# Kernel tuning notes

Hardware: AMD Instinct MI355X
Metric: run time of the kernel (lower is better)

## Reference

```python
import jax, jax.numpy as jnp
import numpy as np

N = 100000
K = 20
SCALES = (5, 10, 20)
D = 256  # dimoffeat


def _leaky(x):
    return jax.nn.leaky_relu(x, negative_slope=0.2)


def setup_inputs() -> dict:
    key = jax.random.key(0)
    ks = jax.random.split(key, 20)
    S = len(SCALES)
    inp = {
        "points": jax.random.normal(ks[0], (N, 3), dtype=jnp.float32),
        "neighbor_indices": jax.random.randint(ks[1], (N, K), 0, N, dtype=jnp.int64),
        # per-scale patch PointNet weights, stacked over the 3 scales
        "pw1": jax.random.normal(ks[2], (S, D // 4, 3), dtype=jnp.float32) * 0.05,
        "pb1": jax.random.normal(ks[3], (S, D // 4), dtype=jnp.float32) * 0.05,
        "pw2": jax.random.normal(ks[4], (S, D // 2, D // 4), dtype=jnp.float32) * 0.05,
        "pb2": jax.random.normal(ks[5], (S, D // 2), dtype=jnp.float32) * 0.05,
        "pw3": jax.random.normal(ks[6], (S, D, D // 2), dtype=jnp.float32) * 0.05,
        "pb3": jax.random.normal(ks[7], (S, D), dtype=jnp.float32) * 0.05,
        # shared MLP (all 1x1 convs == linears)
        "sw1": jax.random.normal(ks[8], (D, S * D), dtype=jnp.float32) * 0.05,
        "sb1": jax.random.normal(ks[9], (D,), dtype=jnp.float32) * 0.05,
        "sw2": jax.random.normal(ks[10], (D // 2, D), dtype=jnp.float32) * 0.05,
        "sb2": jax.random.normal(ks[11], (D // 2,), dtype=jnp.float32) * 0.05,
        "sw3": jax.random.normal(ks[12], (D // 4, D // 2), dtype=jnp.float32) * 0.05,
        "sb3": jax.random.normal(ks[13], (D // 4,), dtype=jnp.float32) * 0.05,
        "sw4": jax.random.normal(ks[14], (D // 8, D // 4), dtype=jnp.float32) * 0.05,
        "sb4": jax.random.normal(ks[15], (D // 8,), dtype=jnp.float32) * 0.05,
        "sw5": jax.random.normal(ks[16], (1, D // 8), dtype=jnp.float32) * 0.05,
        "sb5": jax.random.normal(ks[17], (1,), dtype=jnp.float32) * 0.05,
    }
    return inp


def reference(points, pw1, pb1, pw2, pb2, pw3, pb3,
              sw1, sb1, sw2, sb2, sw3, sb3, sw4, sb4, sw5, sb5,
              neighbor_indices):
    feats_list = []
    for i, s in enumerate(SCALES):
        # gather neighbors and center: [N, s, 3]
        nb = points[neighbor_indices[:, :s]] - points[:, None, :]
        # 1x1-conv MLP == per-point linear layers
        h = _leaky(jnp.einsum('nsc,dc->nsd', nb, pw1[i]) + pb1[i])
        h = _leaky(jnp.einsum('nsc,dc->nsd', h, pw2[i]) + pb2[i])
        h = jnp.einsum('nsc,dc->nsd', h, pw3[i]) + pb3[i]
        feats_list.append(jnp.max(h, axis=1))  # max-pool over neighbors -> [N, D]
    x = jnp.concatenate(feats_list, axis=1)  # [N, 3*D]
    h = _leaky(x @ sw1.T + sb1)
    h = _leaky(h @ sw2.T + sb2)
    h = _leaky(h @ sw3.T + sb3)
    h = _leaky(h @ sw4.T + sb4)
    out = h @ sw5.T + sb5  # [N, 1]
    return out[:, 0]
```

## Files before the change

kernel.cpp:

```cpp
#include <hip/hip_runtime.h>


typedef _Float16 f16x8 __attribute__((ext_vector_type(8)));
typedef _Float16 f16x4 __attribute__((ext_vector_type(4)));
typedef __fp16   h16x2 __attribute__((ext_vector_type(2)));
typedef float    f32x4 __attribute__((ext_vector_type(4)));

#define PPB 32
#define KMAX 20

#define PW2OFF 0
#define PW3OFF 24576
#define SW1OFF 122880
#define SW2OFF 319488
#define SW3OFF 352256
#define SW4OFF 360448
#define NFRAGS 708
#define PW1PAD_BYTES 724992

#define NB_OFF 0
#define H1_OFF 10240
#define H2_OFF 33280
#define PW1S_OFF 76800
#define LDS_BYTES 77824
#define H1S 72
#define H2S 136
#define XIS 264
#define X2S 264
#define H3S 136
#define H4S 72
#define O4S 36

__device__ __forceinline__ float leakyf(float x) { return fmaxf(x, 0.2f * x); }

__device__ __forceinline__ f16x4 pkrtz4(f32x4 a) {
    h16x2 lo = __builtin_amdgcn_cvt_pkrtz(a[0], a[1]);
    h16x2 hi = __builtin_amdgcn_cvt_pkrtz(a[2], a[3]);
    f16x4 r;
    r[0] = (_Float16)lo[0]; r[1] = (_Float16)lo[1];
    r[2] = (_Float16)hi[0]; r[3] = (_Float16)hi[1];
    return r;
}
__device__ __forceinline__ f16x4 leaky4h(f16x4 h) {
    f16x4 s = h * (_Float16)0.2f;
    return __builtin_elementwise_max(h, s);
}
__device__ __forceinline__ f16x4 rne4(f32x4 a) {
    f16x4 r; r[0] = (_Float16)a[0]; r[1] = (_Float16)a[1];
    r[2] = (_Float16)a[2]; r[3] = (_Float16)a[3];
    return r;
}
__device__ __forceinline__ f32x4 ldbias4(const float* b) {
    float4 t = *(const float4*)b;
    return (f32x4){t.x, t.y, t.z, t.w};
}

struct PrepRegion { const float* src; int inC; int Kk; int fEnd; int dstOff; };
struct PrepParams {
    PrepRegion r[10];
    const float* pw1; const float* pb1;
    float* pw1pad; _Float16* dst;
};

__global__ __launch_bounds__(256) void prep_kernel(PrepParams pp) {
    int gid = blockIdx.x * 256 + threadIdx.x;
    if (gid < NFRAGS * 64) {
        int f = gid >> 6, L = gid & 63;
        int ri = 0;
        while (f >= pp.r[ri].fEnd) ri++;
        int f0 = (ri == 0) ? 0 : pp.r[ri - 1].fEnd;
        const PrepRegion R = pp.r[ri];
        int fl = f - f0;
        int nt = fl / R.Kk, kk = fl - nt * R.Kk;
        int row = nt * 16 + (L & 15);
        int col = kk * 32 + (L >> 4) * 8;
        const float* s = R.src + row * R.inC + col;
        f16x8 v;
#pragma unroll
        for (int j = 0; j < 8; ++j) v[j] = (_Float16)s[j];
        *(f16x8*)(pp.dst + R.dstOff + fl * 512 + L * 8) = v;
    } else if (gid < NFRAGS * 64 + 192) {
        int t = gid - NFRAGS * 64;
        int i = t >> 6, fd = t & 63;
        float4 w;
        w.x = pp.pw1[i * 192 + fd * 3 + 0];
        w.y = pp.pw1[i * 192 + fd * 3 + 1];
        w.z = pp.pw1[i * 192 + fd * 3 + 2];
        w.w = pp.pb1[i * 64 + fd];
        ((float4*)pp.pw1pad)[i * 64 + fd] = w;
    }
}

struct MainParams {
    const float* points; const int* nidx;
    const float* pb2; const float* pb3;
    const float* sb1; const float* sb2; const float* sb3; const float* sb4;
    const float* sw5; const float* sb5;
    const _Float16* wsH; const float* pw1pad;
    float* out;
    int n;
};

__global__ __launch_bounds__(256, 2) void msp_mfma(MainParams p) {
    __shared__ __align__(16) unsigned char pool[LDS_BYTES];
    float*    nbf = (float*)(pool + NB_OFF);
    _Float16* h1  = (_Float16*)(pool + H1_OFF);
    _Float16* h2  = (_Float16*)(pool + H2_OFF);
    _Float16* xi  = (_Float16*)(pool + H2_OFF);
    _Float16* x2  = (_Float16*)(pool + H1_OFF);
    _Float16* h3  = (_Float16*)(pool + NB_OFF);
    _Float16* h4  = (_Float16*)(pool + H2_OFF);
    float*    out4= (float*)(pool + H2_OFF + 8192);
    float*    pw1s= (float*)(pool + PW1S_OFF);

    const int tid  = threadIdx.x;
    const int wave = tid >> 6, lane = tid & 63;
    const int q = lane >> 4, m16 = lane & 15;
    const int n0 = blockIdx.x * PPB;

    for (int r = tid; r < PPB * KMAX; r += 256) {
        int pp_ = r & 31, k = r >> 5;
        int idx = p.nidx[(n0 + pp_) * KMAX + k];
        const float* npt = p.points + idx * 3;
        const float* cpt = p.points + (n0 + pp_) * 3;
        float4 v;
        v.x = npt[0] - cpt[0];
        v.y = npt[1] - cpt[1];
        v.z = npt[2] - cpt[2];
        v.w = 1.0f;
        ((float4*)nbf)[r] = v;
    }

    f32x4 accC[2][4];
#pragma unroll
    for (int mt = 0; mt < 4; ++mt) {
        f32x4 b = ldbias4(p.sb1 + (wave * 4 + mt) * 16 + q * 4);
        accC[0][mt] = b; accC[1][mt] = b;
    }
    __syncthreads();

    const int NC[3] = {1, 2, 4};
    for (int i = 0; i < 3; ++i) {
        if (tid < 64)
            ((float4*)pw1s)[tid] = ((const float4*)p.pw1pad)[i * 64 + tid];

        f16x8 W2f[2][2], W3f[4][4];
#pragma unroll
        for (int mt = 0; mt < 2; ++mt)
#pragma unroll
            for (int kk = 0; kk < 2; ++kk)
                W2f[mt][kk] = *(const f16x8*)(p.wsH + PW2OFF +
                    (i * 16 + (wave * 2 + mt) * 2 + kk) * 512 + lane * 8);
#pragma unroll
        for (int mt = 0; mt < 4; ++mt)
#pragma unroll
            for (int kk = 0; kk < 4; ++kk)
                W3f[mt][kk] = *(const f16x8*)(p.wsH + PW3OFF +
                    (i * 64 + (wave * 4 + mt) * 4 + kk) * 512 + lane * 8);

        f32x4 b2v[2];
#pragma unroll
        for (int mt = 0; mt < 2; ++mt)
            b2v[mt] = ldbias4(p.pb2 + i * 128 + (wave * 2 + mt) * 16 + q * 4);

        f32x4 maxC[2][4];
#pragma unroll
        for (int pt = 0; pt < 2; ++pt)
#pragma unroll
            for (int mt = 0; mt < 4; ++mt)
                maxC[pt][mt] = (f32x4){-3.0e38f, -3.0e38f, -3.0e38f, -3.0e38f};

        __syncthreads();

        for (int c = 0; c < NC[i]; ++c) {
            const int k0 = c * 5;
            {
                int p_ = tid & 31, g = tid >> 5;
                for (int kc = 0; kc < 5; ++kc) {
                    float4 nv = ((const float4*)nbf)[(k0 + kc) * 32 + p_];
                    f32x4 v0, v1;
#pragma unroll
                    for (int j = 0; j < 4; ++j) {
                        float4 w = ((const float4*)pw1s)[g * 8 + j];
                        v0[j] = leakyf(fmaf(nv.x, w.x, fmaf(nv.y, w.y, fmaf(nv.z, w.z, w.w))));
                    }
#pragma unroll
                    for (int j = 0; j < 4; ++j) {
                        float4 w = ((const float4*)pw1s)[g * 8 + 4 + j];
                        v1[j] = leakyf(fmaf(nv.x, w.x, fmaf(nv.y, w.y, fmaf(nv.z, w.z, w.w))));
                    }
                    f16x4 a = pkrtz4(v0), b = pkrtz4(v1);
                    f16x8 hv;
#pragma unroll
                    for (int j = 0; j < 4; ++j) { hv[j] = a[j]; hv[4 + j] = b[j]; }
                    *(f16x8*)(h1 + (kc * 32 + p_) * H1S + g * 8) = hv;
                }
            }
            __syncthreads();

            for (int nt = 0; nt < 10; ++nt) {
                const _Float16* br = h1 + (nt * 16 + m16) * H1S + q * 8;
                f16x8 b0 = *(const f16x8*)br;
                f16x8 b1 = *(const f16x8*)(br + 32);
                f32x4 acc0 = __builtin_amdgcn_mfma_f32_16x16x32_f16(W2f[0][0], b0, b2v[0], 0, 0, 0);
                f32x4 acc1 = __builtin_amdgcn_mfma_f32_16x16x32_f16(W2f[1][0], b0, b2v[1], 0, 0, 0);
                acc0 = __builtin_amdgcn_mfma_f32_16x16x32_f16(W2f[0][1], b1, acc0, 0, 0, 0);
                acc1 = __builtin_amdgcn_mfma_f32_16x16x32_f16(W2f[1][1], b1, acc1, 0, 0, 0);
                _Float16* wr = h2 + (nt * 16 + m16) * H2S + q * 4;
                *(f16x4*)(wr + (wave * 2 + 0) * 16) = leaky4h(pkrtz4(acc0));
                *(f16x4*)(wr + (wave * 2 + 1) * 16) = leaky4h(pkrtz4(acc1));
            }
            __syncthreads();

            for (int nt = 0; nt < 10; ++nt) {
                const _Float16* br = h2 + (nt * 16 + m16) * H2S + q * 8;
                f16x8 b[4];
#pragma unroll
                for (int kk = 0; kk < 4; ++kk) b[kk] = *(const f16x8*)(br + kk * 32);
                f32x4 acc[4];
#pragma unroll
                for (int mt = 0; mt < 4; ++mt)
                    acc[mt] = __builtin_amdgcn_mfma_f32_16x16x32_f16(W3f[mt][0], b[0],
                              (f32x4){0.f, 0.f, 0.f, 0.f}, 0, 0, 0);
#pragma unroll
                for (int kk = 1; kk < 4; ++kk)
#pragma unroll
                    for (int mt = 0; mt < 4; ++mt)
                        acc[mt] = __builtin_amdgcn_mfma_f32_16x16x32_f16(W3f[mt][kk], b[kk], acc[mt], 0, 0, 0);
                int pt = nt & 1;
#pragma unroll
                for (int mt = 0; mt < 4; ++mt)
                    maxC[pt][mt] = __builtin_elementwise_max(maxC[pt][mt], acc[mt]);
            }
        }

        __syncthreads();
#pragma unroll
        for (int pt = 0; pt < 2; ++pt)
#pragma unroll
            for (int mt = 0; mt < 4; ++mt) {
                f32x4 b3 = ldbias4(p.pb3 + i * 256 + (wave * 4 + mt) * 16 + q * 4);
                *(f16x4*)(xi + (pt * 16 + m16) * XIS + (wave * 4 + mt) * 16 + q * 4)
                    = rne4(maxC[pt][mt] + b3);
            }
        __syncthreads();

        for (int nt = 0; nt < 2; ++nt) {
            const _Float16* br = xi + (nt * 16 + m16) * XIS + q * 8;
            f16x8 bf[8];
#pragma unroll
            for (int kk = 0; kk < 8; ++kk) bf[kk] = *(const f16x8*)(br + kk * 32);
#pragma unroll
            for (int kk = 0; kk < 8; ++kk)
#pragma unroll
                for (int mt = 0; mt < 4; ++mt) {
                    f16x8 a = *(const f16x8*)(p.wsH + SW1OFF +
                        ((wave * 4 + mt) * 24 + i * 8 + kk) * 512 + lane * 8);
                    accC[nt][mt] = __builtin_amdgcn_mfma_f32_16x16x32_f16(a, bf[kk], accC[nt][mt], 0, 0, 0);
                }
        }
    }

#pragma unroll
    for (int nt = 0; nt < 2; ++nt)
#pragma unroll
        for (int mt = 0; mt < 4; ++mt) {
            f32x4 v = accC[nt][mt];
#pragma unroll
            for (int r = 0; r < 4; ++r) v[r] = leakyf(v[r]);
            *(f16x4*)(x2 + (nt * 16 + m16) * X2S + (wave * 4 + mt) * 16 + q * 4) = rne4(v);
        }
    __syncthreads();

    for (int nt = 0; nt < 2; ++nt) {
        const _Float16* br = x2 + (nt * 16 + m16) * X2S + q * 8;
        f16x8 bf[8];
#pragma unroll
        for (int kk = 0; kk < 8; ++kk) bf[kk] = *(const f16x8*)(br + kk * 32);
        f32x4 acc[2];
#pragma unroll
        for (int mt = 0; mt < 2; ++mt)
            acc[mt] = ldbias4(p.sb2 + (wave * 2 + mt) * 16 + q * 4);
#pragma unroll
        for (int kk = 0; kk < 8; ++kk)
#pragma unroll
            for (int mt = 0; mt < 2; ++mt) {
                f16x8 a = *(const f16x8*)(p.wsH + SW2OFF +
                    ((wave * 2 + mt) * 8 + kk) * 512 + lane * 8);
                acc[mt] = __builtin_amdgcn_mfma_f32_16x16x32_f16(a, bf[kk], acc[mt], 0, 0, 0);
            }
#pragma unroll
        for (int mt = 0; mt < 2; ++mt) {
            f32x4 v = acc[mt];
#pragma unroll
            for (int r = 0; r < 4; ++r) v[r] = leakyf(v[r]);
            *(f16x4*)(h3 + (nt * 16 + m16) * H3S + (wave * 2 + mt) * 16 + q * 4) = rne4(v);
        }
    }
    __syncthreads();

    for (int nt = 0; nt < 2; ++nt) {
        const _Float16* br = h3 + (nt * 16 + m16) * H3S + q * 8;
        f32x4 acc = ldbias4(p.sb3 + wave * 16 + q * 4);
#pragma unroll
        for (int kk = 0; kk < 4; ++kk) {
            f16x8 bf = *(const f16x8*)(br + kk * 32);
            f16x8 a = *(const f16x8*)(p.wsH + SW3OFF + (wave * 4 + kk) * 512 + lane * 8);
            acc = __builtin_amdgcn_mfma_f32_16x16x32_f16(a, bf, acc, 0, 0, 0);
        }
#pragma unroll
        for (int r = 0; r < 4; ++r) acc[r] = leakyf(acc[r]);
        *(f16x4*)(h4 + (nt * 16 + m16) * H4S + wave * 16 + q * 4) = rne4(acc);
    }
    __syncthreads();

    if (wave < 2) {
        for (int nt = 0; nt < 2; ++nt) {
            const _Float16* br = h4 + (nt * 16 + m16) * H4S + q * 8;
            f32x4 acc = ldbias4(p.sb4 + wave * 16 + q * 4);
#pragma unroll
            for (int kk = 0; kk < 2; ++kk) {
                f16x8 bf = *(const f16x8*)(br + kk * 32);
                f16x8 a = *(const f16x8*)(p.wsH + SW4OFF + (wave * 2 + kk) * 512 + lane * 8);
                acc = __builtin_amdgcn_mfma_f32_16x16x32_f16(a, bf, acc, 0, 0, 0);
            }
#pragma unroll
            for (int r = 0; r < 4; ++r) acc[r] = leakyf(acc[r]);
            *(f32x4*)(out4 + (nt * 16 + m16) * O4S + wave * 16 + q * 4) = acc;
        }
    }
    __syncthreads();

    if (tid < PPB) {
        float acc = p.sb5[0];
#pragma unroll
        for (int c = 0; c < 32; ++c)
            acc = fmaf(out4[tid * O4S + c], p.sw5[c], acc);
        p.out[n0 + tid] = acc;
    }
}

extern "C" void kernel_launch(void* const* d_in, const int* in_sizes, int n_in,
                              void* d_out, int out_size, void* d_ws, size_t ws_size,
                              hipStream_t stream) {
    const float* points = (const float*)d_in[0];
    const int*   nidx   = (const int*)d_in[1];
    const float* pw1 = (const float*)d_in[2];  const float* pb1 = (const float*)d_in[3];
    const float* pw2 = (const float*)d_in[4];  const float* pb2 = (const float*)d_in[5];
    const float* pw3 = (const float*)d_in[6];  const float* pb3 = (const float*)d_in[7];
    const float* sw1 = (const float*)d_in[8];  const float* sb1 = (const float*)d_in[9];
    const float* sw2 = (const float*)d_in[10]; const float* sb2 = (const float*)d_in[11];
    const float* sw3 = (const float*)d_in[12]; const float* sb3 = (const float*)d_in[13];
    const float* sw4 = (const float*)d_in[14]; const float* sb4 = (const float*)d_in[15];
    const float* sw5 = (const float*)d_in[16]; const float* sb5 = (const float*)d_in[17];

    _Float16* wsH = (_Float16*)d_ws;
    float* pw1pad = (float*)((char*)d_ws + PW1PAD_BYTES);

    PrepParams pp;
    for (int i = 0; i < 3; ++i)
        pp.r[i] = { pw2 + i * 8192, 64, 2, 16 * (i + 1), PW2OFF + i * 8192 };
    for (int i = 0; i < 3; ++i)
        pp.r[3 + i] = { pw3 + i * 32768, 128, 4, 48 + 64 * (i + 1), PW3OFF + i * 32768 };
    pp.r[6] = { sw1, 768, 24, 624, SW1OFF };
    pp.r[7] = { sw2, 256, 8, 688, SW2OFF };
    pp.r[8] = { sw3, 128, 4, 704, SW3OFF };
    pp.r[9] = { sw4, 64, 2, 708, SW4OFF };
    pp.pw1 = pw1; pp.pb1 = pb1;
    pp.pw1pad = pw1pad; pp.dst = wsH;

    int prep_threads = NFRAGS * 64 + 192;
    hipLaunchKernelGGL(prep_kernel, dim3((prep_threads + 255) / 256), dim3(256), 0, stream, pp);

    MainParams mp;
    mp.points = points; mp.nidx = nidx;
    mp.pb2 = pb2; mp.pb3 = pb3;
    mp.sb1 = sb1; mp.sb2 = sb2; mp.sb3 = sb3; mp.sb4 = sb4;
    mp.sw5 = sw5; mp.sb5 = sb5;
    mp.wsH = wsH; mp.pw1pad = pw1pad;
    mp.out = (float*)d_out;
    mp.n = in_sizes[0] / 3;

    int blocks = mp.n / PPB;
    hipLaunchKernelGGL(msp_mfma, dim3(blocks), dim3(256), 0, stream, mp);
}
```

Before: 439.4 us.

## Halve points per block, compute first layer in packed fp16, raise occupancy

Points per block drop from 32 to 16, which roughly halves LDS use and the accumulator registers, and launch bounds are raised to 3 blocks per CU. The first patch layer is now computed with packed fp16 math from an fp16 copy of the pw1/pb1 weights made in the prep kernel, instead of fp32 FMAs. The aim is better latency hiding through occupancy, at the cost of reloading per-scale weight fragments twice as often per point and lower first-layer precision.

```diff
diff --git a/kernel.cpp b/kernel.cpp
--- a/kernel.cpp
+++ b/kernel.cpp
@@ -3,10 +3,11 @@
 
 typedef _Float16 f16x8 __attribute__((ext_vector_type(8)));
 typedef _Float16 f16x4 __attribute__((ext_vector_type(4)));
+typedef _Float16 f16x2 __attribute__((ext_vector_type(2)));
 typedef __fp16   h16x2 __attribute__((ext_vector_type(2)));
 typedef float    f32x4 __attribute__((ext_vector_type(4)));
 
-#define PPB 32
+#define PPB 16
 #define KMAX 20
 
 #define PW2OFF 0
@@ -15,14 +16,14 @@
 #define SW2OFF 319488
 #define SW3OFF 352256
 #define SW4OFF 360448
+#define PW1HOFF 362496
 #define NFRAGS 708
-#define PW1PAD_BYTES 724992
 
 #define NB_OFF 0
-#define H1_OFF 10240
-#define H2_OFF 33280
-#define PW1S_OFF 76800
-#define LDS_BYTES 77824
+#define H1_OFF 5120
+#define H2_OFF 16640
+#define PW1H_OFF 38400
+#define LDS_BYTES 38912
 #define H1S 72
 #define H2S 136
 #define XIS 264
@@ -59,7 +60,7 @@
 struct PrepParams {
     PrepRegion r[10];
     const float* pw1; const float* pb1;
-    float* pw1pad; _Float16* dst;
+    _Float16* dst;
 };
 
 __global__ __launch_bounds__(256) void prep_kernel(PrepParams pp) {
@@ -79,15 +80,20 @@
 #pragma unroll
         for (int j = 0; j < 8; ++j) v[j] = (_Float16)s[j];
         *(f16x8*)(pp.dst + R.dstOff + fl * 512 + L * 8) = v;
-    } else if (gid < NFRAGS * 64 + 192) {
+    } else if (gid < NFRAGS * 64 + 96) {
         int t = gid - NFRAGS * 64;
-        int i = t >> 6, fd = t & 63;
-        float4 w;
-        w.x = pp.pw1[i * 192 + fd * 3 + 0];
-        w.y = pp.pw1[i * 192 + fd * 3 + 1];
-        w.z = pp.pw1[i * 192 + fd * 3 + 2];
-        w.w = pp.pb1[i * 64 + fd];
-        ((float4*)pp.pw1pad)[i * 64 + fd] = w;
+        int i = t >> 5, pr = t & 31;
+        int c0 = pr * 2, c1 = pr * 2 + 1;
+        f16x8 v;
+        v[0] = (_Float16)pp.pw1[i * 192 + c0 * 3 + 0];
+        v[1] = (_Float16)pp.pw1[i * 192 + c1 * 3 + 0];
+        v[2] = (_Float16)pp.pw1[i * 192 + c0 * 3 + 1];
+        v[3] = (_Float16)pp.pw1[i * 192 + c1 * 3 + 1];
+        v[4] = (_Float16)pp.pw1[i * 192 + c0 * 3 + 2];
+        v[5] = (_Float16)pp.pw1[i * 192 + c1 * 3 + 2];
+        v[6] = (_Float16)pp.pb1[i * 64 + c0];
+        v[7] = (_Float16)pp.pb1[i * 64 + c1];
+        *(f16x8*)(pp.dst + PW1HOFF + (i * 32 + pr) * 8) = v;
     }
 }
 
@@ -96,12 +102,12 @@
     const float* pb2; const float* pb3;
     const float* sb1; const float* sb2; const float* sb3; const float* sb4;
     const float* sw5; const float* sb5;
-    const _Float16* wsH; const float* pw1pad;
+    const _Float16* wsH;
     float* out;
     int n;
 };
 
-__global__ __launch_bounds__(256, 2) void msp_mfma(MainParams p) {
+__global__ __launch_bounds__(256, 3) void msp_mfma(MainParams p) {
     __shared__ __align__(16) unsigned char pool[LDS_BYTES];
     float*    nbf = (float*)(pool + NB_OFF);
     _Float16* h1  = (_Float16*)(pool + H1_OFF);
@@ -110,8 +116,8 @@
     _Float16* x2  = (_Float16*)(pool + H1_OFF);
     _Float16* h3  = (_Float16*)(pool + NB_OFF);
     _Float16* h4  = (_Float16*)(pool + H2_OFF);
-    float*    out4= (float*)(pool + H2_OFF + 8192);
-    float*    pw1s= (float*)(pool + PW1S_OFF);
+    float*    out4= (float*)(pool + H2_OFF + 4096);
+    _Float16* pw1h= (_Float16*)(pool + PW1H_OFF);
 
     const int tid  = threadIdx.x;
     const int wave = tid >> 6, lane = tid & 63;
@@ -119,7 +125,7 @@
     const int n0 = blockIdx.x * PPB;
 
     for (int r = tid; r < PPB * KMAX; r += 256) {
-        int pp_ = r & 31, k = r >> 5;
+        int pp_ = r & 15, k = r >> 4;
         int idx = p.nidx[(n0 + pp_) * KMAX + k];
         const float* npt = p.points + idx * 3;
         const float* cpt = p.points + (n0 + pp_) * 3;
@@ -131,18 +137,16 @@
         ((float4*)nbf)[r] = v;
     }
 
-    f32x4 accC[2][4];
-#pragma unroll
-    for (int mt = 0; mt < 4; ++mt) {
-        f32x4 b = ldbias4(p.sb1 + (wave * 4 + mt) * 16 + q * 4);
-        accC[0][mt] = b; accC[1][mt] = b;
-    }
+    f32x4 accC[4];
+#pragma unroll
+    for (int mt = 0; mt < 4; ++mt)
+        accC[mt] = ldbias4(p.sb1 + (wave * 4 + mt) * 16 + q * 4);
     __syncthreads();
 
     const int NC[3] = {1, 2, 4};
     for (int i = 0; i < 3; ++i) {
-        if (tid < 64)
-            ((float4*)pw1s)[tid] = ((const float4*)p.pw1pad)[i * 64 + tid];
+        if (tid < 32)
+            ((f16x8*)pw1h)[tid] = ((const f16x8*)(p.wsH + PW1HOFF))[i * 32 + tid];
 
         f16x8 W2f[2][2], W3f[4][4];
 #pragma unroll
@@ -163,42 +167,44 @@
         for (int mt = 0; mt < 2; ++mt)
             b2v[mt] = ldbias4(p.pb2 + i * 128 + (wave * 2 + mt) * 16 + q * 4);
 
-        f32x4 maxC[2][4];
-#pragma unroll
-        for (int pt = 0; pt < 2; ++pt)
-#pragma unroll
-            for (int mt = 0; mt < 4; ++mt)
-                maxC[pt][mt] = (f32x4){-3.0e38f, -3.0e38f, -3.0e38f, -3.0e38f};
+        f32x4 maxC[4];
+#pragma unroll
+        for (int mt = 0; mt < 4; ++mt)
+            maxC[mt] = (f32x4){-3.0e38f, -3.0e38f, -3.0e38f, -3.0e38f};
 
         __syncthreads();
 
         for (int c = 0; c < NC[i]; ++c) {
             const int k0 = c * 5;
             {
-                int p_ = tid & 31, g = tid >> 5;
-                for (int kc = 0; kc < 5; ++kc) {
-                    float4 nv = ((const float4*)nbf)[(k0 + kc) * 32 + p_];
-                    f32x4 v0, v1;
-#pragma unroll
-                    for (int j = 0; j < 4; ++j) {
-                        float4 w = ((const float4*)pw1s)[g * 8 + j];
-                        v0[j] = leakyf(fmaf(nv.x, w.x, fmaf(nv.y, w.y, fmaf(nv.z, w.z, w.w))));
+                int p_ = tid & 15;
+                int g  = (tid >> 4) & 7;
+                int kh = tid >> 7;
+                for (int kc = 0; kc < 5; kc += 2) {
+                    int k = kc + kh;
+                    if (k < 5) {
+                        float4 nv = ((const float4*)nbf)[(k0 + k) * 16 + p_];
+                        f16x2 X; X[0] = X[1] = (_Float16)nv.x;
+                        f16x2 Y; Y[0] = Y[1] = (_Float16)nv.y;
+                        f16x2 Z; Z[0] = Z[1] = (_Float16)nv.z;
+                        f16x8 hv;
+#pragma unroll
+                        for (int j = 0; j < 4; ++j) {
+                            f16x8 w8 = ((const f16x8*)pw1h)[g * 4 + j];
+                            f16x2 wx = {w8[0], w8[1]}, wy = {w8[2], w8[3]};
+                            f16x2 wz = {w8[4], w8[5]}, wb = {w8[6], w8[7]};
+                            f16x2 v = wx * X + wy * Y + wz * Z + wb;
+                            f16x2 s = v * (_Float16)0.2f;
+                            v = __builtin_elementwise_max(v, s);
+                            hv[2 * j] = v[0]; hv[2 * j + 1] = v[1];
+                        }
+                        *(f16x8*)(h1 + (k * 16 + p_) * H1S + g * 8) = hv;
                     }
-#pragma unroll
-                    for (int j = 0; j < 4; ++j) {
-                        float4 w = ((const float4*)pw1s)[g * 8 + 4 + j];
-                        v1[j] = leakyf(fmaf(nv.x, w.x, fmaf(nv.y, w.y, fmaf(nv.z, w.z, w.w))));
-                    }
-                    f16x4 a = pkrtz4(v0), b = pkrtz4(v1);
-                    f16x8 hv;
-#pragma unroll
-                    for (int j = 0; j < 4; ++j) { hv[j] = a[j]; hv[4 + j] = b[j]; }
-                    *(f16x8*)(h1 + (kc * 32 + p_) * H1S + g * 8) = hv;
                 }
             }
             __syncthreads();
 
-            for (int nt = 0; nt < 10; ++nt) {
+            for (int nt = 0; nt < 5; ++nt) {
                 const _Float16* br = h1 + (nt * 16 + m16) * H1S + q * 8;
                 f16x8 b0 = *(const f16x8*)br;
                 f16x8 b1 = *(const f16x8*)(br + 32);
@@ -212,7 +218,7 @@
             }
             __syncthreads();
 
-            for (int nt = 0; nt < 10; ++nt) {
+            for (int nt = 0; nt < 5; ++nt) {
                 const _Float16* br = h2 + (nt * 16 + m16) * H2S + q * 8;
                 f16x8 b[4];
 #pragma unroll
@@ -227,26 +233,23 @@
 #pragma unroll
                     for (int mt = 0; mt < 4; ++mt)
                         acc[mt] = __builtin_amdgcn_mfma_f32_16x16x32_f16(W3f[mt][kk], b[kk], acc[mt], 0, 0, 0);
-                int pt = nt & 1;
 #pragma unroll
                 for (int mt = 0; mt < 4; ++mt)
-                    maxC[pt][mt] = __builtin_elementwise_max(maxC[pt][mt], acc[mt]);
+                    maxC[mt] = __builtin_elementwise_max(maxC[mt], acc[mt]);
             }
         }
 
         __syncthreads();
 #pragma unroll
-        for (int pt = 0; pt < 2; ++pt)
-#pragma unroll
-            for (int mt = 0; mt < 4; ++mt) {
-                f32x4 b3 = ldbias4(p.pb3 + i * 256 + (wave * 4 + mt) * 16 + q * 4);
-                *(f16x4*)(xi + (pt * 16 + m16) * XIS + (wave * 4 + mt) * 16 + q * 4)
-                    = rne4(maxC[pt][mt] + b3);
-            }
+        for (int mt = 0; mt < 4; ++mt) {
+            f32x4 b3 = ldbias4(p.pb3 + i * 256 + (wave * 4 + mt) * 16 + q * 4);
+            *(f16x4*)(xi + m16 * XIS + (wave * 4 + mt) * 16 + q * 4)
+                = rne4(maxC[mt] + b3);
+        }
         __syncthreads();
 
-        for (int nt = 0; nt < 2; ++nt) {
-            const _Float16* br = xi + (nt * 16 + m16) * XIS + q * 8;
+        {
+            const _Float16* br = xi + m16 * XIS + q * 8;
             f16x8 bf[8];
 #pragma unroll
             for (int kk = 0; kk < 8; ++kk) bf[kk] = *(const f16x8*)(br + kk * 32);
@@ -256,24 +259,22 @@
                 for (int mt = 0; mt < 4; ++mt) {
                     f16x8 a = *(const f16x8*)(p.wsH + SW1OFF +
                         ((wave * 4 + mt) * 24 + i * 8 + kk) * 512 + lane * 8);
-                    accC[nt][mt] = __builtin_amdgcn_mfma_f32_16x16x32_f16(a, bf[kk], accC[nt][mt], 0, 0, 0);
+                    accC[mt] = __builtin_amdgcn_mfma_f32_16x16x32_f16(a, bf[kk], accC[mt], 0, 0, 0);
                 }
         }
     }
 
 #pragma unroll
-    for (int nt = 0; nt < 2; ++nt)
-#pragma unroll
-        for (int mt = 0; mt < 4; ++mt) {
-            f32x4 v = accC[nt][mt];
-#pragma unroll
-            for (int r = 0; r < 4; ++r) v[r] = leakyf(v[r]);
-            *(f16x4*)(x2 + (nt * 16 + m16) * X2S + (wave * 4 + mt) * 16 + q * 4) = rne4(v);
-        }
-    __syncthreads();
-
-    for (int nt = 0; nt < 2; ++nt) {
-        const _Float16* br = x2 + (nt * 16 + m16) * X2S + q * 8;
+    for (int mt = 0; mt < 4; ++mt) {
+        f32x4 v = accC[mt];
+#pragma unroll
+        for (int r = 0; r < 4; ++r) v[r] = leakyf(v[r]);
+        *(f16x4*)(x2 + m16 * X2S + (wave * 4 + mt) * 16 + q * 4) = rne4(v);
+    }
+    __syncthreads();
+
+    {
+        const _Float16* br = x2 + m16 * X2S + q * 8;
         f16x8 bf[8];
 #pragma unroll
         for (int kk = 0; kk < 8; ++kk) bf[kk] = *(const f16x8*)(br + kk * 32);
@@ -294,13 +295,13 @@
             f32x4 v = acc[mt];
 #pragma unroll
             for (int r = 0; r < 4; ++r) v[r] = leakyf(v[r]);
-            *(f16x4*)(h3 + (nt * 16 + m16) * H3S + (wave * 2 + mt) * 16 + q * 4) = rne4(v);
-        }
-    }
-    __syncthreads();
-
-    for (int nt = 0; nt < 2; ++nt) {
-        const _Float16* br = h3 + (nt * 16 + m16) * H3S + q * 8;
+            *(f16x4*)(h3 + m16 * H3S + (wave * 2 + mt) * 16 + q * 4) = rne4(v);
+        }
+    }
+    __syncthreads();
+
+    {
+        const _Float16* br = h3 + m16 * H3S + q * 8;
         f32x4 acc = ldbias4(p.sb3 + wave * 16 + q * 4);
 #pragma unroll
         for (int kk = 0; kk < 4; ++kk) {
@@ -310,24 +311,22 @@
         }
 #pragma unroll
         for (int r = 0; r < 4; ++r) acc[r] = leakyf(acc[r]);
-        *(f16x4*)(h4 + (nt * 16 + m16) * H4S + wave * 16 + q * 4) = rne4(acc);
+        *(f16x4*)(h4 + m16 * H4S + wave * 16 + q * 4) = rne4(acc);
     }
     __syncthreads();
 
     if (wave < 2) {
-        for (int nt = 0; nt < 2; ++nt) {
-            const _Float16* br = h4 + (nt * 16 + m16) * H4S + q * 8;
-            f32x4 acc = ldbias4(p.sb4 + wave * 16 + q * 4);
-#pragma unroll
-            for (int kk = 0; kk < 2; ++kk) {
-                f16x8 bf = *(const f16x8*)(br + kk * 32);
-                f16x8 a = *(const f16x8*)(p.wsH + SW4OFF + (wave * 2 + kk) * 512 + lane * 8);
-                acc = __builtin_amdgcn_mfma_f32_16x16x32_f16(a, bf, acc, 0, 0, 0);
-            }
-#pragma unroll
-            for (int r = 0; r < 4; ++r) acc[r] = leakyf(acc[r]);
-            *(f32x4*)(out4 + (nt * 16 + m16) * O4S + wave * 16 + q * 4) = acc;
-        }
+        const _Float16* br = h4 + m16 * H4S + q * 8;
+        f32x4 acc = ldbias4(p.sb4 + wave * 16 + q * 4);
+#pragma unroll
+        for (int kk = 0; kk < 2; ++kk) {
+            f16x8 bf = *(const f16x8*)(br + kk * 32);
+            f16x8 a = *(const f16x8*)(p.wsH + SW4OFF + (wave * 2 + kk) * 512 + lane * 8);
+            acc = __builtin_amdgcn_mfma_f32_16x16x32_f16(a, bf, acc, 0, 0, 0);
+        }
+#pragma unroll
+        for (int r = 0; r < 4; ++r) acc[r] = leakyf(acc[r]);
+        *(f32x4*)(out4 + m16 * O4S + wave * 16 + q * 4) = acc;
     }
     __syncthreads();
 
@@ -355,7 +354,6 @@
     const float* sw5 = (const float*)d_in[16]; const float* sb5 = (const float*)d_in[17];
 
     _Float16* wsH = (_Float16*)d_ws;
-    float* pw1pad = (float*)((char*)d_ws + PW1PAD_BYTES);
 
     PrepParams pp;
     for (int i = 0; i < 3; ++i)
@@ -367,9 +365,9 @@
     pp.r[8] = { sw3, 128, 4, 704, SW3OFF };
     pp.r[9] = { sw4, 64, 2, 708, SW4OFF };
     pp.pw1 = pw1; pp.pb1 = pb1;
-    pp.pw1pad = pw1pad; pp.dst = wsH;
-
-    int prep_threads = NFRAGS * 64 + 192;
+    pp.dst = wsH;
+
+    int prep_threads = NFRAGS * 64 + 96;
     hipLaunchKernelGGL(prep_kernel, dim3((prep_threads + 255) / 256), dim3(256), 0, stream, pp);
 
     MainParams mp;
@@ -377,7 +375,7 @@
     mp.pb2 = pb2; mp.pb3 = pb3;
     mp.sb1 = sb1; mp.sb2 = sb2; mp.sb3 = sb3; mp.sb4 = sb4;
     mp.sw5 = sw5; mp.sb5 = sb5;
-    mp.wsH = wsH; mp.pw1pad = pw1pad;
+    mp.wsH = wsH;
     mp.out = (float*)d_out;
     mp.n = in_sizes[0] / 3;
 
```

Measured after the change: 533.0 us. 21.3% more time.

## Compute first patch layer in packed fp16 and pad LDS strides

Applied to the files above, without the earlier changes.

The first per-point layer (3-to-64 linear plus leaky ReLU) is now computed with packed half2 arithmetic. Its weights and bias are pre-converted to fp16 and interleaved per channel pair in the prep kernel, replacing the fp32 FMA path and the pack conversion. LDS row strides for all intermediate buffers are also padded by 8 bytes, which changes bank mapping and grows the LDS footprint slightly. The fp16 arithmetic on the first layer reduces accuracy, and the larger LDS use could affect occupancy.

```diff
diff --git a/kernel.cpp b/kernel.cpp
--- a/kernel.cpp
+++ b/kernel.cpp
@@ -3,6 +3,7 @@
 
 typedef _Float16 f16x8 __attribute__((ext_vector_type(8)));
 typedef _Float16 f16x4 __attribute__((ext_vector_type(4)));
+typedef _Float16 f16x2 __attribute__((ext_vector_type(2)));
 typedef __fp16   h16x2 __attribute__((ext_vector_type(2)));
 typedef float    f32x4 __attribute__((ext_vector_type(4)));
 
@@ -15,20 +16,20 @@
 #define SW2OFF 319488
 #define SW3OFF 352256
 #define SW4OFF 360448
+#define PW1HOFF 362496
 #define NFRAGS 708
-#define PW1PAD_BYTES 724992
 
 #define NB_OFF 0
 #define H1_OFF 10240
-#define H2_OFF 33280
-#define PW1S_OFF 76800
-#define LDS_BYTES 77824
-#define H1S 72
-#define H2S 136
-#define XIS 264
-#define X2S 264
-#define H3S 136
-#define H4S 72
+#define H2_OFF 34560
+#define PW1H_OFF 79360
+#define LDS_BYTES 79872
+#define H1S 76
+#define H2S 140
+#define XIS 268
+#define X2S 268
+#define H3S 140
+#define H4S 76
 #define O4S 36
 
 __device__ __forceinline__ float leakyf(float x) { return fmaxf(x, 0.2f * x); }
@@ -59,7 +60,7 @@
 struct PrepParams {
     PrepRegion r[10];
     const float* pw1; const float* pb1;
-    float* pw1pad; _Float16* dst;
+    _Float16* dst;
 };
 
 __global__ __launch_bounds__(256) void prep_kernel(PrepParams pp) {
@@ -79,15 +80,20 @@
 #pragma unroll
         for (int j = 0; j < 8; ++j) v[j] = (_Float16)s[j];
         *(f16x8*)(pp.dst + R.dstOff + fl * 512 + L * 8) = v;
-    } else if (gid < NFRAGS * 64 + 192) {
+    } else if (gid < NFRAGS * 64 + 96) {
         int t = gid - NFRAGS * 64;
-        int i = t >> 6, fd = t & 63;
-        float4 w;
-        w.x = pp.pw1[i * 192 + fd * 3 + 0];
-        w.y = pp.pw1[i * 192 + fd * 3 + 1];
-        w.z = pp.pw1[i * 192 + fd * 3 + 2];
-        w.w = pp.pb1[i * 64 + fd];
-        ((float4*)pp.pw1pad)[i * 64 + fd] = w;
+        int i = t >> 5, pr = t & 31;
+        int c0 = pr * 2, c1 = pr * 2 + 1;
+        f16x8 v;
+        v[0] = (_Float16)pp.pw1[i * 192 + c0 * 3 + 0];
+        v[1] = (_Float16)pp.pw1[i * 192 + c1 * 3 + 0];
+        v[2] = (_Float16)pp.pw1[i * 192 + c0 * 3 + 1];
+        v[3] = (_Float16)pp.pw1[i * 192 + c1 * 3 + 1];
+        v[4] = (_Float16)pp.pw1[i * 192 + c0 * 3 + 2];
+        v[5] = (_Float16)pp.pw1[i * 192 + c1 * 3 + 2];
+        v[6] = (_Float16)pp.pb1[i * 64 + c0];
+        v[7] = (_Float16)pp.pb1[i * 64 + c1];
+        *(f16x8*)(pp.dst + PW1HOFF + (i * 32 + pr) * 8) = v;
     }
 }
 
@@ -96,7 +102,7 @@
     const float* pb2; const float* pb3;
     const float* sb1; const float* sb2; const float* sb3; const float* sb4;
     const float* sw5; const float* sb5;
-    const _Float16* wsH; const float* pw1pad;
+    const _Float16* wsH;
     float* out;
     int n;
 };
@@ -111,7 +117,7 @@
     _Float16* h3  = (_Float16*)(pool + NB_OFF);
     _Float16* h4  = (_Float16*)(pool + H2_OFF);
     float*    out4= (float*)(pool + H2_OFF + 8192);
-    float*    pw1s= (float*)(pool + PW1S_OFF);
+    _Float16* pw1h= (_Float16*)(pool + PW1H_OFF);
 
     const int tid  = threadIdx.x;
     const int wave = tid >> 6, lane = tid & 63;
@@ -141,8 +147,8 @@
 
     const int NC[3] = {1, 2, 4};
     for (int i = 0; i < 3; ++i) {
-        if (tid < 64)
-            ((float4*)pw1s)[tid] = ((const float4*)p.pw1pad)[i * 64 + tid];
+        if (tid < 32)
+            ((f16x8*)pw1h)[tid] = ((const f16x8*)(p.wsH + PW1HOFF))[i * 32 + tid];
 
         f16x8 W2f[2][2], W3f[4][4];
 #pragma unroll
@@ -176,23 +182,23 @@
             const int k0 = c * 5;
             {
                 int p_ = tid & 31, g = tid >> 5;
+#pragma unroll
                 for (int kc = 0; kc < 5; ++kc) {
                     float4 nv = ((const float4*)nbf)[(k0 + kc) * 32 + p_];
-                    f32x4 v0, v1;
+                    f16x2 X; X[0] = X[1] = (_Float16)nv.x;
+                    f16x2 Y; Y[0] = Y[1] = (_Float16)nv.y;
+                    f16x2 Z; Z[0] = Z[1] = (_Float16)nv.z;
+                    f16x8 hv;
 #pragma unroll
                     for (int j = 0; j < 4; ++j) {
-                        float4 w = ((const float4*)pw1s)[g * 8 + j];
-                        v0[j] = leakyf(fmaf(nv.x, w.x, fmaf(nv.y, w.y, fmaf(nv.z, w.z, w.w))));
+                        f16x8 w8 = ((const f16x8*)pw1h)[g * 4 + j];
+                        f16x2 wx = {w8[0], w8[1]}, wy = {w8[2], w8[3]};
+                        f16x2 wz = {w8[4], w8[5]}, wb = {w8[6], w8[7]};
+                        f16x2 v = wx * X + wy * Y + wz * Z + wb;
+                        f16x2 s = v * (_Float16)0.2f;
+                        v = __builtin_elementwise_max(v, s);
+                        hv[2 * j] = v[0]; hv[2 * j + 1] = v[1];
                     }
-#pragma unroll
-                    for (int j = 0; j < 4; ++j) {
-                        float4 w = ((const float4*)pw1s)[g * 8 + 4 + j];
-                        v1[j] = leakyf(fmaf(nv.x, w.x, fmaf(nv.y, w.y, fmaf(nv.z, w.z, w.w))));
-                    }
-                    f16x4 a = pkrtz4(v0), b = pkrtz4(v1);
-                    f16x8 hv;
-#pragma unroll
-                    for (int j = 0; j < 4; ++j) { hv[j] = a[j]; hv[4 + j] = b[j]; }
                     *(f16x8*)(h1 + (kc * 32 + p_) * H1S + g * 8) = hv;
                 }
             }
@@ -355,7 +361,6 @@
     const float* sw5 = (const float*)d_in[16]; const float* sb5 = (const float*)d_in[17];
 
     _Float16* wsH = (_Float16*)d_ws;
-    float* pw1pad = (float*)((char*)d_ws + PW1PAD_BYTES);
 
     PrepParams pp;
     for (int i = 0; i < 3; ++i)
@@ -367,9 +372,9 @@
     pp.r[8] = { sw3, 128, 4, 704, SW3OFF };
     pp.r[9] = { sw4, 64, 2, 708, SW4OFF };
     pp.pw1 = pw1; pp.pb1 = pb1;
-    pp.pw1pad = pw1pad; pp.dst = wsH;
-
-    int prep_threads = NFRAGS * 64 + 192;
+    pp.dst = wsH;
+
+    int prep_threads = NFRAGS * 64 + 96;
     hipLaunchKernelGGL(prep_kernel, dim3((prep_threads + 255) / 256), dim3(256), 0, stream, pp);
 
     MainParams mp;
@@ -377,7 +382,7 @@
     mp.pb2 = pb2; mp.pb3 = pb3;
     mp.sb1 = sb1; mp.sb2 = sb2; mp.sb3 = sb3; mp.sb4 = sb4;
     mp.sw5 = sw5; mp.sb5 = sb5;
-    mp.wsH = wsH; mp.pw1pad = pw1pad;
+    mp.wsH = wsH;
     mp.out = (float*)d_out;
     mp.n = in_sizes[0] / 3;
 
```

Measured after the change: 893.7 us. 103% more time.
